# Kernel optimization log

Measured on AMD Instinct MI355X. Metric: run time of the kernel, lower is better.

Reference implementation:

```python
import jax, jax.numpy as jnp
import numpy as np

PR = np.float32(0.7)
RA = np.float32(1e6)
LAM_DATA = 1.0
LAM_TB = 1.0
LAM_CONTI = 1.0
LAM_NSE = 1.0
LAM_EE = 1.0


def _act(a):
    return 0.5 * jnp.sin(2.0 * jnp.pi * a)


def _mlp(x, W_in, b_in, W_hid, b_hid, W_out, b_out):
    # x: (..., 4) -> (..., 4); 6 hidden layers of width D, sin activation
    h = _act(x @ W_in + b_in)
    for i in range(W_hid.shape[0]):  # static small loop over hidden layers
        h = _act(h @ W_hid[i] + b_hid[i])
    return h @ W_out + b_out


def setup_inputs() -> dict:
    key = jax.random.key(0)
    ks = jax.random.split(key, 6)
    N, D = 4096, 128
    inputs = jax.random.uniform(ks[0], (N, 4), dtype=jnp.float32)
    y_true = jax.random.normal(ks[1], (N, 4), dtype=jnp.float32)
    W_in = jax.random.normal(ks[2], (4, D), dtype=jnp.float32) / jnp.sqrt(4.0)
    b_in = jnp.zeros((D,), jnp.float32)
    W_hid = jax.random.normal(ks[3], (5, D, D), dtype=jnp.float32) / jnp.sqrt(float(D))
    b_hid = jnp.zeros((5, D), jnp.float32)
    W_out = jax.random.normal(ks[4], (D, 4), dtype=jnp.float32) / jnp.sqrt(float(D))
    b_out = jnp.zeros((4,), jnp.float32)
    return {"inputs": inputs, "y_true": y_true, "W_in": W_in, "b_in": b_in,
            "W_hid": W_hid, "b_hid": b_hid, "W_out": W_out, "b_out": b_out}


def reference(inputs, y_true, W_in, b_in, W_hid, b_hid, W_out, b_out):
    # input order: (t, x, y, z) = indices (0,1,2,3); output order: (u, v, w, T)
    f = lambda xi: _mlp(xi, W_in, b_in, W_hid, b_hid, W_out, b_out)  # R^4 -> R^4
    y_pred = _mlp(inputs, W_in, b_in, W_hid, b_hid, W_out, b_out)    # (N,4)
    # Per-point derivative tensors via nested forward-mode (replaces ~30 tape.gradient calls)
    J = jax.vmap(jax.jacfwd(f))(inputs)                               # (N, out, d1)
    H = jax.vmap(jax.jacfwd(jax.jacfwd(f)))(inputs)                   # (N, out, d1, d2)
    G3 = jax.vmap(jax.jacfwd(jax.jacfwd(jax.jacfwd(f))))(inputs)      # (N, out, d1, d2, d3)

    u, v, w = y_pred[:, 0], y_pred[:, 1], y_pred[:, 2]
    u_x, u_y, u_z = J[:, 0, 1], J[:, 0, 2], J[:, 0, 3]
    v_x, v_y, v_z = J[:, 1, 1], J[:, 1, 2], J[:, 1, 3]
    w_x, w_y, w_z = J[:, 2, 1], J[:, 2, 2], J[:, 2, 3]
    T_t, T_x, T_y, T_z = J[:, 3, 0], J[:, 3, 1], J[:, 3, 2], J[:, 3, 3]

    s = jnp.sqrt(PR / RA)
    kappa = np.float32(np.sqrt(1.0 / (0.7 * 1e6)))

    # data loss: MSE over (u,v,w)
    loss_data = jnp.mean(jnp.square(y_pred[:, :3] - y_true[:, :3]))

    # temperature boundary loss at z in {0,1}
    N = inputs.shape[0]
    kb1, kb2 = jax.random.split(jax.random.key(22))
    xy_b = jax.random.uniform(kb1, (N, 2), dtype=inputs.dtype)
    z_b = jax.random.randint(kb2, (N, 1), 0, 2).astype(inputs.dtype)
    inp_b = jnp.concatenate([inputs[:, :1], xy_b, z_b], axis=1)
    T_b = _mlp(inp_b, W_in, b_in, W_hid, b_hid, W_out, b_out)[:, 3]
    T_true_b = jnp.where(z_b[:, 0] == 0.0, 0.5, -0.5)  # T_max at z=0, T_min at z=1
    loss_Tb = jnp.mean(jnp.square(T_true_b - T_b))

    # continuity
    loss_conti = jnp.mean(jnp.square(u_x + v_y + w_z))

    # vorticity-form NSE residuals
    NSE_u = (H[:, 2, 2, 0] - H[:, 1, 3, 0]
             + u * (H[:, 2, 2, 1] - H[:, 1, 3, 1])
             + v * (H[:, 2, 2, 2] - H[:, 1, 3, 2])
             + w * (H[:, 2, 2, 3] - H[:, 1, 3, 3])
             - (w_y - v_z) * u_x - (u_z - w_x) * u_y - (v_x - u_y) * u_z
             - s * (G3[:, 2, 2, 1, 1] - G3[:, 1, 3, 1, 1]
                    + G3[:, 2, 2, 2, 2] - G3[:, 1, 3, 2, 2]
                    + G3[:, 2, 2, 3, 3] - G3[:, 1, 3, 3, 3])
             - T_y)
    NSE_v = (H[:, 0, 3, 0] - H[:, 2, 1, 0]
             + u * (H[:, 0, 3, 1] - H[:, 2, 1, 1])
             + v * (H[:, 0, 3, 2] - H[:, 2, 1, 2])
             + w * (H[:, 0, 3, 3] - H[:, 2, 1, 3])
             - (w_y - v_z) * v_x - (u_z - w_x) * v_y - (v_x - u_y) * v_z
             - s * (G3[:, 0, 3, 1, 1] - G3[:, 2, 1, 1, 1]
                    + G3[:, 0, 3, 2, 2] - G3[:, 2, 1, 2, 2]
                    + G3[:, 0, 3, 3, 3] - G3[:, 2, 1, 3, 3])
             + T_x)
    NSE_w = (H[:, 1, 1, 0] - H[:, 0, 2, 0]
             + u * (H[:, 1, 1, 1] - H[:, 0, 2, 1])
             + v * (H[:, 1, 1, 2] - H[:, 0, 2, 2])
             + w * (H[:, 1, 1, 3] - H[:, 0, 2, 3])
             - (w_y - v_z) * w_x - (u_z - w_x) * w_y - (v_x - u_y) * w_z
             - s * (G3[:, 1, 1, 1, 1] - G3[:, 0, 2, 1, 1]
                    + G3[:, 1, 1, 2, 2] - G3[:, 0, 2, 2, 2]
                    + G3[:, 1, 1, 3, 3] - G3[:, 0, 2, 3, 3]))
    loss_NSE = jnp.mean(jnp.square(jnp.stack([NSE_u, NSE_v, NSE_w])))

    # energy equation
    EE = T_t + u * T_x + v * T_y + w * T_z - kappa * (H[:, 3, 1, 1] + H[:, 3, 2, 2] + H[:, 3, 3, 3])
    loss_EE = jnp.mean(jnp.square(EE))

    total = (LAM_DATA * loss_data + LAM_CONTI * loss_conti + LAM_NSE * loss_NSE
             + LAM_EE * loss_EE + LAM_TB * loss_Tb)
    return total
```

## Files before the change

kernel.cpp:

```cpp
#include <hip/hip_runtime.h>
#include <math.h>

#define NPTS 4096
#define DD   128
#define NCH  24
#define NHID 5
#define PPB  4
#define BS   256
#define WP8  17
#define WPW  68
#define PLSZ 26112
#define OSM_OFF 52224
#define ROWM(p,c) (16*((c)>>2) + 4*(p) + ((c)&3))

typedef __attribute__((ext_vector_type(8))) _Float16 half8;
typedef __attribute__((ext_vector_type(4))) float f32x4;

#define SS_INV 1024.0f
#define ST_INV 65536.0f

static __device__ __forceinline__ unsigned short f2h_bits(float x) {
  _Float16 h = (_Float16)x; unsigned short u; __builtin_memcpy(&u, &h, 2); return u;
}
static __device__ __forceinline__ float h2f(unsigned short u) {
  _Float16 h; __builtin_memcpy(&h, &u, 2); return (float)h;
}
static __device__ __forceinline__ unsigned pk2(float a, float b) {
  return (unsigned)f2h_bits(a) | ((unsigned)f2h_bits(b) << 16);
}

static __device__ __forceinline__ void tf2x32(unsigned k0, unsigned k1,
                                              unsigned x0, unsigned x1,
                                              unsigned &o0, unsigned &o1) {
  unsigned ks2 = 0x1BD11BDAu ^ k0 ^ k1;
  x0 += k0; x1 += k1;
#define TFR(r) { x0 += x1; x1 = (x1 << (r)) | (x1 >> (32 - (r))); x1 ^= x0; }
  TFR(13) TFR(15) TFR(26) TFR(6)  x0 += k1;  x1 += ks2 + 1u;
  TFR(17) TFR(29) TFR(16) TFR(24) x0 += ks2; x1 += k0 + 2u;
  TFR(13) TFR(15) TFR(26) TFR(6)  x0 += k0;  x1 += k1 + 3u;
  TFR(17) TFR(29) TFR(16) TFR(24) x0 += k1;  x1 += ks2 + 4u;
  TFR(13) TFR(15) TFR(26) TFR(6)  x0 += ks2; x1 += k0 + 5u;
#undef TFR
  o0 = x0; o1 = x1;
}
static __device__ __forceinline__ float bits_to_unif(unsigned b) {
  return __uint_as_float((b >> 9) | 0x3f800000u) - 1.0f;
}
static __device__ __forceinline__ void bnd_rand(int pt, float &xb1, float &xb2,
                                                unsigned &zbit) {
  unsigned a0, a1, b0, b1;
  tf2x32(0u, 22u, 0u, 2u, a0, b0);
  tf2x32(0u, 22u, 1u, 3u, a1, b1);
  unsigned f0, f1, zf, o0_, o1_;
  unsigned jj0 = 2u * (unsigned)pt, jj1 = jj0 + 1u;
  if (jj0 < 4096u) { tf2x32(a0, a1, jj0,         jj0 + 4096u, o0_, o1_); f0 = o0_; }
  else             { tf2x32(a0, a1, jj0 - 4096u, jj0,         o0_, o1_); f0 = o1_; }
  if (jj1 < 4096u) { tf2x32(a0, a1, jj1,         jj1 + 4096u, o0_, o1_); f1 = o0_; }
  else             { tf2x32(a0, a1, jj1 - 4096u, jj1,         o0_, o1_); f1 = o1_; }
  if (pt < 2048)   { tf2x32(b0, b1, (unsigned)pt,         (unsigned)pt + 2048u, o0_, o1_); zf = o0_; }
  else             { tf2x32(b0, b1, (unsigned)pt - 2048u, (unsigned)pt,         o0_, o1_); zf = o1_; }
  xb1 = bits_to_unif(f0); xb2 = bits_to_unif(f1); zbit = zf & 1u;
}

static __device__ __forceinline__ void activate_jet(float q[NCH]) {
  const float PI1 = 3.14159265358979323846f;
  float hr = q[0] - floorf(q[0]);
  float sv = __builtin_amdgcn_sinf(hr);
  float cv = __builtin_amdgcn_cosf(hr);
  float p1 = PI1 * cv;
  float p2  = -2.0f * PI1 * PI1 * sv;
  float p3  = -4.0f * PI1 * PI1 * PI1 * cv;
  float p2s = p2 * 9.765625e-4f;
  float p2t = p2 * 0.015625f;
  float p3t = p3 * 1.52587890625e-5f;
  float g0 = q[1], g1 = q[2], g2 = q[3], g3 = q[4];
  float s_tx = q[5], s_ty = q[6], s_tz = q[7], s_xx = q[8], s_xy = q[9],
        s_xz = q[10], s_yy = q[11], s_yz = q[12], s_zz = q[13];
  float T0 = q[14], T1 = q[15], T2 = q[16], T3 = q[17], T4 = q[18],
        T5 = q[19], T6 = q[20], T7 = q[21], T8 = q[22];
  q[0] = 0.5f * sv;
  q[1] = p1 * g0; q[2] = p1 * g1; q[3] = p1 * g2; q[4] = p1 * g3;
  q[5]  = p2s * g0 * g1 + p1 * s_tx;
  q[6]  = p2s * g0 * g2 + p1 * s_ty;
  q[7]  = p2s * g0 * g3 + p1 * s_tz;
  q[8]  = p2s * g1 * g1 + p1 * s_xx;
  q[9]  = p2s * g1 * g2 + p1 * s_xy;
  q[10] = p2s * g1 * g3 + p1 * s_xz;
  q[11] = p2s * g2 * g2 + p1 * s_yy;
  q[12] = p2s * g2 * g3 + p1 * s_yz;
  q[13] = p2s * g3 * g3 + p1 * s_zz;
  q[14] = p3t * g1 * g1 * g1 + p2t * (3.0f * s_xx * g1)              + p1 * T0;
  q[15] = p3t * g2 * g1 * g1 + p2t * (2.0f * s_xy * g1 + s_xx * g2)  + p1 * T1;
  q[16] = p3t * g3 * g1 * g1 + p2t * (2.0f * s_xz * g1 + s_xx * g3)  + p1 * T2;
  q[17] = p3t * g1 * g2 * g2 + p2t * (2.0f * s_xy * g2 + s_yy * g1)  + p1 * T3;
  q[18] = p3t * g2 * g2 * g2 + p2t * (3.0f * s_yy * g2)              + p1 * T4;
  q[19] = p3t * g3 * g2 * g2 + p2t * (2.0f * s_yz * g2 + s_yy * g3)  + p1 * T5;
  q[20] = p3t * g1 * g3 * g3 + p2t * (2.0f * s_xz * g3 + s_zz * g1)  + p1 * T6;
  q[21] = p3t * g2 * g3 * g3 + p2t * (2.0f * s_yz * g3 + s_zz * g2)  + p1 * T7;
  q[22] = p3t * g3 * g3 * g3 + p2t * (3.0f * s_zz * g3)              + p1 * T8;
  float br = q[23] - floorf(q[23]);
  q[23] = 0.5f * __builtin_amdgcn_sinf(br);
}

__global__ __launch_bounds__(256) void prep_kernel(
    const float* __restrict__ W_hid, const float* __restrict__ W_out,
    unsigned short* __restrict__ wshi, unsigned short* __restrict__ wslo,
    unsigned short* __restrict__ aohi, unsigned short* __restrict__ aolo,
    float4* __restrict__ rnd, float* __restrict__ out) {
  int b = blockIdx.x;
  if (b == 0 && threadIdx.x == 0) out[0] = 0.0f;
  if (b < 320) {
    int idx = b * 256 + threadIdx.x;
    int l = idx >> 14, r = idx & 16383;
    int nt = r >> 11, r2 = r & 2047;
    int ks = r2 >> 9, r3 = r2 & 511;
    int nl = r3 >> 5, r4 = r3 & 31;
    int quad = r4 >> 3, e = r4 & 7;
    int jin  = 32 * ks + 16 * (e & 1) + 4 * quad + (e >> 1);
    int jout = nt * 16 + nl;
    float w = W_hid[(l << 14) + (jin << 7) + jout];
    unsigned short hi = f2h_bits(w);
    wshi[idx] = hi; wslo[idx] = f2h_bits(w - h2f(hi));
  } else if (b < 328) {
    int idx = (b - 320) * 256 + threadIdx.x;
    int ks = idx >> 9, r3 = idx & 511;
    int nl = r3 >> 5, r4 = r3 & 31;
    int quad = r4 >> 3, e = r4 & 7;
    int jin = 32 * ks + 16 * (e & 1) + 4 * quad + (e >> 1);
    float w = (nl < 4) ? W_out[jin * 4 + nl] : 0.0f;
    unsigned short hi = f2h_bits(w);
    aohi[idx] = hi; aolo[idx] = f2h_bits(w - h2f(hi));
  } else {
    int pt = (b - 328) * 256 + threadIdx.x;
    float xb1, xb2; unsigned zbit;
    bnd_rand(pt, xb1, xb2, zbit);
    rnd[pt] = make_float4(xb1, xb2, (float)zbit, zbit ? -0.5f : 0.5f);
  }
}

__global__ __launch_bounds__(BS, 3) void pinn_kernel(
    const float* __restrict__ inputs, const float* __restrict__ y_true,
    const float* __restrict__ W_in,  const float* __restrict__ b_in,
    const float* __restrict__ b_hid, const float* __restrict__ b_out,
    const unsigned short* __restrict__ wshi,
    const unsigned short* __restrict__ wslo,
    const unsigned short* __restrict__ aohi,
    const unsigned short* __restrict__ aolo,
    const float4* __restrict__ rnd,
    float* __restrict__ out)
{
  __shared__ __align__(16) unsigned char smem[53760];
  _Float16* plane0 = (_Float16*)smem;
  _Float16* plane1 = (_Float16*)(smem + PLSZ);
  float* Osm = (float*)(smem + OSM_OFF);

  const int t    = threadIdx.x;
  const int wave = t >> 6;
  const int lane = t & 63;
  const int q    = lane >> 4;
  const int nl   = lane & 15;
  const int P    = 16 * wave + nl;
  const int ja   = 32 * wave + nl;
  const int jb   = ja + 16;
  const int pt0  = blockIdx.x * PPB;

  {
    const int p1 = t >> 6;
    const int P1 = lane;
    const int j1a = 32 * (P1 >> 4) + (P1 & 15), j1b = j1a + 16;
    const int pt = pt0 + p1;
    float4 rv = rnd[pt];
    float x_t = inputs[pt * 4 + 0], x_x = inputs[pt * 4 + 1];
    float x_y = inputs[pt * 4 + 2], x_z = inputs[pt * 4 + 3];
    float q0[NCH], q1[NCH];
#pragma unroll
    for (int h = 0; h < 2; ++h) {
      int jj = h ? j1b : j1a;
      float* qq = h ? q1 : q0;
      float w0 = W_in[0 * DD + jj], w1 = W_in[1 * DD + jj],
            w2 = W_in[2 * DD + jj], w3 = W_in[3 * DD + jj];
      float bb = b_in[jj];
      qq[0] = bb + x_t * w0 + x_x * w1 + x_y * w2 + x_z * w3;
      qq[1] = w0; qq[2] = w1; qq[3] = w2; qq[4] = w3;
#pragma unroll
      for (int c = 5; c < 23; ++c) qq[c] = 0.0f;
      qq[23] = bb + x_t * w0 + rv.x * w1 + rv.y * w2 + rv.z * w3;
      activate_jet(qq);
    }
    unsigned* dw = (unsigned*)plane0;
#pragma unroll
    for (int c = 0; c < NCH; ++c)
      dw[ROWM(p1, c) * WPW + P1] = pk2(q0[c], q1[c]);
  }
  __syncthreads();

  const half8* wh8 = (const half8*)wshi;
  const half8* wl8 = (const half8*)wslo;
  for (int l = 0; l < NHID; ++l) {
    const half8* src = (const half8*)((l & 1) ? plane1 : plane0);
    unsigned* dstw = (unsigned*)((l & 1) ? plane0 : plane1);

    f32x4 acc[6][2];
#pragma unroll
    for (int mt = 0; mt < 6; ++mt) { acc[mt][0] = (f32x4)0.0f; acc[mt][1] = (f32x4)0.0f; }

#pragma unroll
    for (int ks = 0; ks < 4; ++ks) {
      half8 a[6], bh[2], bl[2];
#pragma unroll
      for (int mt = 0; mt < 6; ++mt)
        a[mt] = src[(16 * mt + nl) * WP8 + ks * 4 + q];
#pragma unroll
      for (int i = 0; i < 2; ++i) {
        int bi = ((l * 8 + 2 * wave + i) * 4 + ks) * 64 + nl * 4 + q;
        bh[i] = wh8[bi]; bl[i] = wl8[bi];
      }
#pragma unroll
      for (int mt = 0; mt < 6; ++mt)
#pragma unroll
        for (int i = 0; i < 2; ++i) {
          acc[mt][i] = __builtin_amdgcn_mfma_f32_16x16x32_f16(a[mt], bh[i], acc[mt][i], 0, 0, 0);
          acc[mt][i] = __builtin_amdgcn_mfma_f32_16x16x32_f16(a[mt], bl[i], acc[mt][i], 0, 0, 0);
        }
    }

    float qa[NCH], qb[NCH];
#pragma unroll
    for (int mt = 0; mt < 6; ++mt)
#pragma unroll
      for (int r = 0; r < 4; ++r) {
        qa[4 * mt + r] = acc[mt][0][r];
        qb[4 * mt + r] = acc[mt][1][r];
      }
    float ba = b_hid[l * DD + ja], bb_ = b_hid[l * DD + jb];
    qa[0] += ba; qa[23] += ba;
    qb[0] += bb_; qb[23] += bb_;
    activate_jet(qa);
    activate_jet(qb);
#pragma unroll
    for (int c = 0; c < NCH; ++c)
      dstw[ROWM(q, c) * WPW + P] = pk2(qa[c], qb[c]);
    __syncthreads();
  }

  {
    const half8* src = (const half8*)plane1;
    const half8* oh8 = (const half8*)aohi;
    const half8* ol8 = (const half8*)aolo;
    if (wave < 3) {
      f32x4 acc2[2];
      acc2[0] = (f32x4)0.0f; acc2[1] = (f32x4)0.0f;
#pragma unroll
      for (int ks = 0; ks < 4; ++ks) {
        half8 a0 = src[(16 * (2 * wave)     + nl) * WP8 + ks * 4 + q];
        half8 a1 = src[(16 * (2 * wave + 1) + nl) * WP8 + ks * 4 + q];
        int bi = ks * 64 + nl * 4 + q;
        half8 oh = oh8[bi], ol = ol8[bi];
        acc2[0] = __builtin_amdgcn_mfma_f32_16x16x32_f16(a0, oh, acc2[0], 0, 0, 0);
        acc2[0] = __builtin_amdgcn_mfma_f32_16x16x32_f16(a0, ol, acc2[0], 0, 0, 0);
        acc2[1] = __builtin_amdgcn_mfma_f32_16x16x32_f16(a1, oh, acc2[1], 0, 0, 0);
        acc2[1] = __builtin_amdgcn_mfma_f32_16x16x32_f16(a1, ol, acc2[1], 0, 0, 0);
      }
      if (nl < 4) {
#pragma unroll
        for (int i = 0; i < 2; ++i)
#pragma unroll
          for (int r = 0; r < 4; ++r)
            Osm[(q * NCH + 4 * (2 * wave + i) + r) * 4 + nl] = acc2[i][r];
      }
    }
  }
  __syncthreads();

  if (t < PPB) {
    const int pp = t;
    const int ptt = pt0 + pp;
    const float Ttrue = rnd[ptt].w;
    const float SEC  = SS_INV;
    const float SCT  = 8.36660026534e-04f * ST_INV;
    const float KAPS = 1.19522860933e-03f * SS_INV;
    float bo0 = b_out[0], bo1 = b_out[1], bo2 = b_out[2], bo3 = b_out[3];
#define OO(o, c) Osm[(pp * NCH + (c)) * 4 + (o)]
    float u  = OO(0, 0) + bo0, v_ = OO(1, 0) + bo1, w_ = OO(2, 0) + bo2;
    float ux = OO(0, 2), uy = OO(0, 3), uz = OO(0, 4);
    float vx = OO(1, 2), vy = OO(1, 3), vz = OO(1, 4);
    float wx = OO(2, 2), wy = OO(2, 3), wz = OO(2, 4);
    float Tt = OO(3, 1), Tx = OO(3, 2), Ty = OO(3, 3), Tz = OO(3, 4);

    float hu = OO(2, 6) - OO(1, 7)
             + u  * (OO(2, 9)  - OO(1, 10))
             + v_ * (OO(2, 11) - OO(1, 12))
             + w_ * (OO(2, 12) - OO(1, 13));
    float NSEu = SEC * hu
               - (wy - vz) * ux - (uz - wx) * uy - (vx - uy) * uz
               - SCT * (OO(2, 15) - OO(1, 16) + OO(2, 18) - OO(1, 19) + OO(2, 21) - OO(1, 22))
               - Ty;
    float hv = OO(0, 7) - OO(2, 5)
             + u  * (OO(0, 10) - OO(2, 8))
             + v_ * (OO(0, 12) - OO(2, 9))
             + w_ * (OO(0, 13) - OO(2, 10));
    float NSEv = SEC * hv
               - (wy - vz) * vx - (uz - wx) * vy - (vx - uy) * vz
               - SCT * (OO(0, 16) - OO(2, 14) + OO(0, 19) - OO(2, 17) + OO(0, 22) - OO(2, 20))
               + Tx;
    float hw = OO(1, 5) - OO(0, 6)
             + u  * (OO(1, 8)  - OO(0, 9))
             + v_ * (OO(1, 9)  - OO(0, 11))
             + w_ * (OO(1, 10) - OO(0, 12));
    float NSEw = SEC * hw
               - (wy - vz) * wx - (uz - wx) * wy - (vx - uy) * wz
               - SCT * (OO(1, 14) - OO(0, 15) + OO(1, 17) - OO(0, 18) + OO(1, 20) - OO(0, 21));

    float EE = Tt + u * Tx + v_ * Ty + w_ * Tz
             - KAPS * (OO(3, 8) + OO(3, 11) + OO(3, 13));

    float conti = ux + vy + wz;
    const float* yt = y_true + ptt * 4;
    float d0 = u - yt[0], d1 = v_ - yt[1], d2 = w_ - yt[2];
    float dT = Ttrue - (OO(3, 23) + bo3);
#undef OO
    const float invN  = 1.0f / (float)NPTS;
    const float inv3N = 1.0f / (3.0f * (float)NPTS);
    float part = (d0 * d0 + d1 * d1 + d2 * d2) * inv3N
               + conti * conti * invN
               + (NSEu * NSEu + NSEv * NSEv + NSEw * NSEw) * inv3N
               + EE * EE * invN
               + dT * dT * invN;
    atomicAdd(out, part);
  }
}

extern "C" void kernel_launch(void* const* d_in, const int* in_sizes, int n_in,
                              void* d_out, int out_size, void* d_ws, size_t ws_size,
                              hipStream_t stream) {
  const float* inputs = (const float*)d_in[0];
  const float* y_true = (const float*)d_in[1];
  const float* W_in   = (const float*)d_in[2];
  const float* b_in   = (const float*)d_in[3];
  const float* W_hid  = (const float*)d_in[4];
  const float* b_hid  = (const float*)d_in[5];
  const float* W_out  = (const float*)d_in[6];
  const float* b_out  = (const float*)d_in[7];
  float* out = (float*)d_out;

  unsigned char* ws = (unsigned char*)d_ws;
  unsigned short* wshi = (unsigned short*)(ws);
  unsigned short* wslo = (unsigned short*)(ws + 163840);
  unsigned short* aohi = (unsigned short*)(ws + 327680);
  unsigned short* aolo = (unsigned short*)(ws + 331776);
  float4*         rnd  = (float4*)(ws + 335872);

  prep_kernel<<<344, 256, 0, stream>>>(W_hid, W_out, wshi, wslo, aohi, aolo,
                                       rnd, out);
  pinn_kernel<<<NPTS / PPB, BS, 0, stream>>>(inputs, y_true, W_in, b_in,
                                             b_hid, b_out,
                                             wshi, wslo, aohi, aolo, rnd, out);
}
```

Measured before the change: 116.1 us.

## Drop fp16 lo-weight split, prefetch next-layer weights into registers, use pkrtz packing

Removes the hi/lo fp16 weight split, so each hidden-layer and output GEMM issues half as many MFMAs and loads half the weight bytes. Weights for the next layer are prefetched into a double-buffered register array while the current layer computes, and the loop is fully unrolled. Jet packing now uses the packed round-toward-zero conversion instruction. Weight precision drops to plain fp16, which affects accuracy of the third-derivative terms, and the register arrays add pressure.

```diff
diff --git a/kernel.cpp b/kernel.cpp
--- a/kernel.cpp
+++ b/kernel.cpp
@@ -14,6 +14,7 @@
 #define ROWM(p,c) (16*((c)>>2) + 4*(p) + ((c)&3))
 
 typedef __attribute__((ext_vector_type(8))) _Float16 half8;
+typedef __attribute__((ext_vector_type(2))) __fp16 fp16x2;
 typedef __attribute__((ext_vector_type(4))) float f32x4;
 
 #define SS_INV 1024.0f
@@ -22,11 +23,9 @@
 static __device__ __forceinline__ unsigned short f2h_bits(float x) {
   _Float16 h = (_Float16)x; unsigned short u; __builtin_memcpy(&u, &h, 2); return u;
 }
-static __device__ __forceinline__ float h2f(unsigned short u) {
-  _Float16 h; __builtin_memcpy(&h, &u, 2); return (float)h;
-}
 static __device__ __forceinline__ unsigned pk2(float a, float b) {
-  return (unsigned)f2h_bits(a) | ((unsigned)f2h_bits(b) << 16);
+  fp16x2 h = __builtin_amdgcn_cvt_pkrtz(a, b);
+  unsigned u; __builtin_memcpy(&u, &h, 4); return u;
 }
 
 static __device__ __forceinline__ void tf2x32(unsigned k0, unsigned k1,
@@ -104,8 +103,7 @@
 
 __global__ __launch_bounds__(256) void prep_kernel(
     const float* __restrict__ W_hid, const float* __restrict__ W_out,
-    unsigned short* __restrict__ wshi, unsigned short* __restrict__ wslo,
-    unsigned short* __restrict__ aohi, unsigned short* __restrict__ aolo,
+    unsigned short* __restrict__ wsh, unsigned short* __restrict__ aoh,
     float4* __restrict__ rnd, float* __restrict__ out) {
   int b = blockIdx.x;
   if (b == 0 && threadIdx.x == 0) out[0] = 0.0f;
@@ -118,18 +116,14 @@
     int quad = r4 >> 3, e = r4 & 7;
     int jin  = 32 * ks + 16 * (e & 1) + 4 * quad + (e >> 1);
     int jout = nt * 16 + nl;
-    float w = W_hid[(l << 14) + (jin << 7) + jout];
-    unsigned short hi = f2h_bits(w);
-    wshi[idx] = hi; wslo[idx] = f2h_bits(w - h2f(hi));
+    wsh[idx] = f2h_bits(W_hid[(l << 14) + (jin << 7) + jout]);
   } else if (b < 328) {
     int idx = (b - 320) * 256 + threadIdx.x;
     int ks = idx >> 9, r3 = idx & 511;
     int nl = r3 >> 5, r4 = r3 & 31;
     int quad = r4 >> 3, e = r4 & 7;
     int jin = 32 * ks + 16 * (e & 1) + 4 * quad + (e >> 1);
-    float w = (nl < 4) ? W_out[jin * 4 + nl] : 0.0f;
-    unsigned short hi = f2h_bits(w);
-    aohi[idx] = hi; aolo[idx] = f2h_bits(w - h2f(hi));
+    aoh[idx] = f2h_bits((nl < 4) ? W_out[jin * 4 + nl] : 0.0f);
   } else {
     int pt = (b - 328) * 256 + threadIdx.x;
     float xb1, xb2; unsigned zbit;
@@ -142,10 +136,8 @@
     const float* __restrict__ inputs, const float* __restrict__ y_true,
     const float* __restrict__ W_in,  const float* __restrict__ b_in,
     const float* __restrict__ b_hid, const float* __restrict__ b_out,
-    const unsigned short* __restrict__ wshi,
-    const unsigned short* __restrict__ wslo,
-    const unsigned short* __restrict__ aohi,
-    const unsigned short* __restrict__ aolo,
+    const unsigned short* __restrict__ wsh,
+    const unsigned short* __restrict__ aoh,
     const float4* __restrict__ rnd,
     float* __restrict__ out)
 {
@@ -164,6 +156,16 @@
   const int jb   = ja + 16;
   const int pt0  = blockIdx.x * PPB;
 
+  const half8* wh8 = (const half8*)wsh;
+  const half8* oh8 = (const half8*)aoh;
+
+  half8 wr[2][8];
+#pragma unroll
+  for (int z = 0; z < 8; ++z) {
+    int i = z >> 2, ks = z & 3;
+    wr[0][z] = wh8[((2 * wave + i) * 4 + ks) * 64 + nl * 4 + q];
+  }
+
   {
     const int p1 = t >> 6;
     const int P1 = lane;
@@ -194,8 +196,7 @@
   }
   __syncthreads();
 
-  const half8* wh8 = (const half8*)wshi;
-  const half8* wl8 = (const half8*)wslo;
+#pragma unroll
   for (int l = 0; l < NHID; ++l) {
     const half8* src = (const half8*)((l & 1) ? plane1 : plane0);
     unsigned* dstw = (unsigned*)((l & 1) ? plane0 : plane1);
@@ -206,22 +207,23 @@
 
 #pragma unroll
     for (int ks = 0; ks < 4; ++ks) {
-      half8 a[6], bh[2], bl[2];
+      half8 a[6];
 #pragma unroll
       for (int mt = 0; mt < 6; ++mt)
         a[mt] = src[(16 * mt + nl) * WP8 + ks * 4 + q];
 #pragma unroll
-      for (int i = 0; i < 2; ++i) {
-        int bi = ((l * 8 + 2 * wave + i) * 4 + ks) * 64 + nl * 4 + q;
-        bh[i] = wh8[bi]; bl[i] = wl8[bi];
+      for (int mt = 0; mt < 6; ++mt)
+#pragma unroll
+        for (int i = 0; i < 2; ++i)
+          acc[mt][i] = __builtin_amdgcn_mfma_f32_16x16x32_f16(a[mt], wr[l & 1][i * 4 + ks], acc[mt][i], 0, 0, 0);
+    }
+
+    if (l + 1 < NHID) {
+#pragma unroll
+      for (int z = 0; z < 8; ++z) {
+        int i = z >> 2, ks = z & 3;
+        wr[(l + 1) & 1][z] = wh8[(((l + 1) * 8 + 2 * wave + i) * 4 + ks) * 64 + nl * 4 + q];
       }
-#pragma unroll
-      for (int mt = 0; mt < 6; ++mt)
-#pragma unroll
-        for (int i = 0; i < 2; ++i) {
-          acc[mt][i] = __builtin_amdgcn_mfma_f32_16x16x32_f16(a[mt], bh[i], acc[mt][i], 0, 0, 0);
-          acc[mt][i] = __builtin_amdgcn_mfma_f32_16x16x32_f16(a[mt], bl[i], acc[mt][i], 0, 0, 0);
-        }
     }
 
     float qa[NCH], qb[NCH];
@@ -245,8 +247,6 @@
 
   {
     const half8* src = (const half8*)plane1;
-    const half8* oh8 = (const half8*)aohi;
-    const half8* ol8 = (const half8*)aolo;
     if (wave < 3) {
       f32x4 acc2[2];
       acc2[0] = (f32x4)0.0f; acc2[1] = (f32x4)0.0f;
@@ -254,12 +254,9 @@
       for (int ks = 0; ks < 4; ++ks) {
         half8 a0 = src[(16 * (2 * wave)     + nl) * WP8 + ks * 4 + q];
         half8 a1 = src[(16 * (2 * wave + 1) + nl) * WP8 + ks * 4 + q];
-        int bi = ks * 64 + nl * 4 + q;
-        half8 oh = oh8[bi], ol = ol8[bi];
+        half8 oh = oh8[ks * 64 + nl * 4 + q];
         acc2[0] = __builtin_amdgcn_mfma_f32_16x16x32_f16(a0, oh, acc2[0], 0, 0, 0);
-        acc2[0] = __builtin_amdgcn_mfma_f32_16x16x32_f16(a0, ol, acc2[0], 0, 0, 0);
         acc2[1] = __builtin_amdgcn_mfma_f32_16x16x32_f16(a1, oh, acc2[1], 0, 0, 0);
-        acc2[1] = __builtin_amdgcn_mfma_f32_16x16x32_f16(a1, ol, acc2[1], 0, 0, 0);
       }
       if (nl < 4) {
 #pragma unroll
@@ -344,15 +341,11 @@
   float* out = (float*)d_out;
 
   unsigned char* ws = (unsigned char*)d_ws;
-  unsigned short* wshi = (unsigned short*)(ws);
-  unsigned short* wslo = (unsigned short*)(ws + 163840);
-  unsigned short* aohi = (unsigned short*)(ws + 327680);
-  unsigned short* aolo = (unsigned short*)(ws + 331776);
-  float4*         rnd  = (float4*)(ws + 335872);
-
-  prep_kernel<<<344, 256, 0, stream>>>(W_hid, W_out, wshi, wslo, aohi, aolo,
-                                       rnd, out);
+  unsigned short* wsh = (unsigned short*)(ws);
+  unsigned short* aoh = (unsigned short*)(ws + 163840);
+  float4*         rnd = (float4*)(ws + 167936);
+
+  prep_kernel<<<344, 256, 0, stream>>>(W_hid, W_out, wsh, aoh, rnd, out);
   pinn_kernel<<<NPTS / PPB, BS, 0, stream>>>(inputs, y_true, W_in, b_in,
-                                             b_hid, b_out,
-                                             wshi, wslo, aohi, aolo, rnd, out);
-}
+                                             b_hid, b_out, wsh, aoh, rnd, out);
+}
```

New measurement: 95.65 us (median of 4 runs). -17.6%, faster.
